# Kernel tuning notes

Hardware: AMD Instinct MI355X
Metric: run time of the kernel (lower is better)

Reference implementation:

```python
import jax, jax.numpy as jnp
import numpy as np

B, T, F, H = 64, 2048, 64, 160


def setup_inputs() -> dict:
    key = jax.random.key(0)
    ks = jax.random.split(key, 20)
    s = lambda *shape: 0.05
    inp = {
        "x": jax.random.normal(ks[0], (B, T, F), jnp.float32),
        # dilated conv weight [out=F, in=F, k=3]
        "mix_w": jax.random.normal(ks[1], (F, F, 3), jnp.float32) * 0.1,
        # batchnorm (inference) params
        "bn_g": jnp.ones((F,), jnp.float32),
        "bn_b": jnp.zeros((F,), jnp.float32),
        "bn_m": jax.random.normal(ks[2], (F,), jnp.float32) * 0.1,
        "bn_v": jax.random.uniform(ks[3], (F,), jnp.float32, 0.5, 1.5),
        # GRU1: input F -> hidden H (pytorch gate order r, z, n)
        "w_ih1": jax.random.normal(ks[4], (3 * H, F), jnp.float32) * 0.05,
        "w_hh1": jax.random.normal(ks[5], (3 * H, H), jnp.float32) * 0.05,
        "b_ih1": jax.random.normal(ks[6], (3 * H,), jnp.float32) * 0.05,
        "b_hh1": jax.random.normal(ks[7], (3 * H,), jnp.float32) * 0.05,
        # GRU2: hidden H -> hidden H
        "w_ih2": jax.random.normal(ks[8], (3 * H, H), jnp.float32) * 0.05,
        "w_hh2": jax.random.normal(ks[9], (3 * H, H), jnp.float32) * 0.05,
        "b_ih2": jax.random.normal(ks[10], (3 * H,), jnp.float32) * 0.05,
        "b_hh2": jax.random.normal(ks[11], (3 * H,), jnp.float32) * 0.05,
        # head: Linear(H, H//2) -> GELU -> (dropout=identity in eval) -> Linear(H//2, 2)
        "hw1": jax.random.normal(ks[12], (H // 2, H), jnp.float32) * 0.05,
        "hb1": jnp.zeros((H // 2,), jnp.float32),
        "hw2": jax.random.normal(ks[13], (2, H // 2), jnp.float32) * 0.05,
        "hb2": jnp.zeros((2,), jnp.float32),
    }
    return inp


def _gru(z, w_ih, w_hh, b_ih, b_hh):
    # z: [B, T, in]; returns (all hidden states [B, T, H], final hidden [B, H])
    xg = jnp.einsum('bti,gi->btg', z, w_ih) + b_ih  # [B, T, 3H]
    xg = xg.transpose(1, 0, 2)                       # [T, B, 3H]
    h0 = jnp.zeros((z.shape[0], w_hh.shape[1]), z.dtype)

    def step(h, g):
        hg = h @ w_hh.T + b_hh
        xr, xz, xn = jnp.split(g, 3, axis=-1)
        hr, hz, hn = jnp.split(hg, 3, axis=-1)
        r = jax.nn.sigmoid(xr + hr)
        u = jax.nn.sigmoid(xz + hz)
        n = jnp.tanh(xn + r * hn)
        h_new = (1.0 - u) * n + u * h
        return h_new, h_new

    hT, hs = jax.lax.scan(step, h0, xg)
    return hs.transpose(1, 0, 2), hT


def reference(x, mix_w, bn_g, bn_b, bn_m, bn_v,
              w_ih1, w_hh1, b_ih1, b_hh1,
              w_ih2, w_hh2, b_ih2, b_hh2,
              hw1, hb1, hw2, hb2):
    # dilated conv over time: x [B,T,F] -> [B,F,T]
    xc = x.transpose(0, 2, 1)
    y = jax.lax.conv_general_dilated(
        xc, mix_w, window_strides=(1,), padding=[(2, 2)],
        rhs_dilation=(2,), dimension_numbers=('NCH', 'OIH', 'NCH'))
    # batchnorm (inference) + exact GELU
    scale = bn_g / jnp.sqrt(bn_v + 1e-5)
    y = (y - bn_m[:, None]) * scale[:, None] + bn_b[:, None]
    z = jax.nn.gelu(y, approximate=False).transpose(0, 2, 1)  # [B,T,F]

    h1, _ = _gru(z, w_ih1, w_hh1, b_ih1, b_hh1)    # [B,T,H]
    _, h2T = _gru(h1, w_ih2, w_hh2, b_ih2, b_hh2)  # [B,H] (last timestep)

    q = jax.nn.gelu(h2T @ hw1.T + hb1, approximate=False)
    return q @ hw2.T + hb2  # [B, 2]
```

## Files before the change

### kernel.cpp

```cpp
#include <hip/hip_runtime.h>
#include <cmath>

#define BB 64
#define TT 2048
#define FF 64
#define HH 160
#define G3 480
#define TC 128
#define NC (TT / TC)

#define L2E  1.44269504088896340736f
#define TL2E 2.88539008177792681472f

typedef unsigned int u32;
typedef _Float16 half8 __attribute__((ext_vector_type(8)));
typedef _Float16 half2v __attribute__((ext_vector_type(2)));
typedef float f32x4 __attribute__((ext_vector_type(4)));

__device__ __forceinline__ unsigned short f2h(float v) {
    _Float16 h = (_Float16)v;
    return __builtin_bit_cast(unsigned short, h);
}
__device__ __forceinline__ u32 packh2(float a, float b) {
    return (u32)f2h(a) | ((u32)f2h(b) << 16);
}
__device__ __forceinline__ u32 packhh(_Float16 a, _Float16 b) {
    return (u32)__builtin_bit_cast(unsigned short, a)
         | ((u32)__builtin_bit_cast(unsigned short, b) << 16);
}
__device__ __forceinline__ float h2sel(u32 p, u32 sh) {
    return (float)__builtin_bit_cast(half2v, p >> sh)[0];
}
__device__ __forceinline__ float frcp(float v) { return __builtin_amdgcn_rcpf(v); }
#if __has_builtin(__builtin_amdgcn_exp2f)
__device__ __forceinline__ float fexp2(float v) { return __builtin_amdgcn_exp2f(v); }
#else
__device__ __forceinline__ float fexp2(float v) { return __expf(v * 0.69314718055994530942f); }
#endif
__device__ __forceinline__ float gelu_exact(float v) {
    return 0.5f * v * (1.f + erff(v * 0.70710678118654752f));
}
__device__ __forceinline__ void barrier_lgkm() {
    asm volatile("s_waitcnt lgkmcnt(0)\ns_barrier" ::: "memory");
}
__device__ __forceinline__ half8 load_wrow8s(const float* p, float s) {
    const float4* q = (const float4*)p;
    float4 a = q[0], b = q[1];
    half8 r;
    r[0] = (_Float16)(a.x * s); r[1] = (_Float16)(a.y * s);
    r[2] = (_Float16)(a.z * s); r[3] = (_Float16)(a.w * s);
    r[4] = (_Float16)(b.x * s); r[5] = (_Float16)(b.y * s);
    r[6] = (_Float16)(b.z * s); r[7] = (_Float16)(b.w * s);
    return r;
}
__device__ __forceinline__ void split8(const float* v, half8& hi, half8& lo) {
    #pragma unroll
    for (int j = 0; j < 8; ++j) {
        _Float16 h = (_Float16)v[j];
        hi[j] = h;
        lo[j] = (_Float16)(v[j] - (float)h);
    }
}
#define MM16(A_, B_, C_) __builtin_amdgcn_mfma_f32_16x16x32_f16(A_, B_, C_, 0, 0, 0)

__global__ __launch_bounds__(256) void conv_mfma_kernel(
    const float* __restrict__ x, const float* __restrict__ mix_w,
    const float* __restrict__ bn_g, const float* __restrict__ bn_b,
    const float* __restrict__ bn_m, const float* __restrict__ bn_v,
    u32* __restrict__ z_out)
{
    __shared__ __align__(16) u32 xs[68 * 68];
    __shared__ __align__(8)  u32 zt[16 * 34];

    const int b   = blockIdx.y;
    const int t0  = blockIdx.x * 64;
    const int tid = threadIdx.x;
    const int wv = tid >> 6;
    const int lane = tid & 63;
    const int lane15 = lane & 15;
    const int quad = lane >> 4;

    {
        const float* xb = x + (size_t)b * TT * FF;
        for (int idx = tid; idx < 68 * 32; idx += 256) {
            const int row = idx >> 5;
            const int fp  = (idx & 31) * 2;
            const int t = t0 - 2 + row;
            float v0 = 0.f, v1 = 0.f;
            if (t >= 0 && t < TT) {
                float2 v = *(const float2*)(xb + (size_t)t * FF + fp);
                v0 = v.x; v1 = v.y;
            }
            _Float16 h0 = (_Float16)v0, h1 = (_Float16)v1;
            _Float16 l0 = (_Float16)(v0 - (float)h0);
            _Float16 l1 = (_Float16)(v1 - (float)h1);
            u32* rw = xs + row * 68;
            rw[(fp >> 1)]      = packhh(h0, h1);
            rw[32 + (fp >> 1)] = packhh(l0, l1);
        }
    }

    half8 Ahi[6], Alo[6];
    {
        const int fo = wv * 16 + lane15;
        const float* wrow = mix_w + fo * 192;
        #pragma unroll
        for (int s = 0; s < 6; ++s) {
            float wf[8];
            #pragma unroll
            for (int j = 0; j < 8; ++j) {
                int kap = s * 32 + quad * 8 + j;
                wf[j] = wrow[(kap & 63) * 3 + (kap >> 6)];
            }
            split8(wf, Ahi[s], Alo[s]);
        }
    }
    float sc[4], sh[4];
    #pragma unroll
    for (int r = 0; r < 4; ++r) {
        int f = wv * 16 + quad * 4 + r;
        float scl = bn_g[f] * rsqrtf(bn_v[f] + 1e-5f);
        sc[r] = scl; sh[r] = bn_b[f] - bn_m[f] * scl;
    }

    __syncthreads();

    u32* zrow = z_out + (size_t)(b >> 4) * TT * 512 + (b & 15) * 32;
    const int srow = tid >> 4;
    const int sc2  = tid & 15;

    for (int tt = 0; tt < 4; ++tt) {
        f32x4 C = {0.f, 0.f, 0.f, 0.f};
        #pragma unroll
        for (int s = 0; s < 6; ++s) {
            const int row = tt * 16 + lane15 + 2 * (s >> 1);
            const u32* rp = xs + row * 68 + (s & 1) * 16 + quad * 4;
            half8 Bhi = __builtin_bit_cast(half8, *(const uint4*)(rp));
            half8 Blo = __builtin_bit_cast(half8, *(const uint4*)(rp + 32));
            C = MM16(Ahi[s], Bhi, C);
            C = MM16(Ahi[s], Blo, C);
            C = MM16(Alo[s], Bhi, C);
        }
        float z0 = gelu_exact(fmaf(C[0], sc[0], sh[0]));
        float z1 = gelu_exact(fmaf(C[1], sc[1], sh[1]));
        float z2 = gelu_exact(fmaf(C[2], sc[2], sh[2]));
        float z3 = gelu_exact(fmaf(C[3], sc[3], sh[3]));
        const u32 q0 = packh2(z0, z1);
        const u32 q1 = packh2(z2, z3);
        __syncthreads();
        *(uint2*)(zt + lane15 * 34 + wv * 8 + quad * 2) = (uint2){q0, q1};
        __syncthreads();
        uint2 v = *(const uint2*)(zt + srow * 34 + sc2 * 2);
        *(uint2*)(zrow + (size_t)(t0 + tt * 16 + srow) * 512 + sc2 * 2) = v;
    }
}

#define DECLAI(i) half8 A##i##_0, A##i##_1, A##i##_2, A##i##_3, A##i##_4;
#define GLOADA(i) { int tl = wv4 + (i); int rowc = tl < 30 ? tl * 16 + lane15 : 479; \
    float sA = tl < 20 ? L2E : TL2E;                                                 \
    const float* wp = W + (size_t)rowc * K + quad * 8;                               \
    A##i##_0 = load_wrow8s(wp, sA); A##i##_1 = load_wrow8s(wp + 32, sA);             \
    if (KT > 2) { A##i##_2 = load_wrow8s(wp + 64, sA);                               \
                  A##i##_3 = load_wrow8s(wp + 96, sA);                               \
                  A##i##_4 = load_wrow8s(wp + 128, sA); }                            \
    else { A##i##_2 = A##i##_0; A##i##_3 = A##i##_0; A##i##_4 = A##i##_0; } }
#define GMM(i, kt) C##i = MM16(A##i##_##kt, Bk##kt, C##i);

template<int K, int KT, int TG>
__device__ __forceinline__ void gemm_body(
    const unsigned short* __restrict__ in,
    size_t in_blk_stride, int t_off,
    const float* __restrict__ W, const float* __restrict__ b_ih,
    const float* __restrict__ b_hh, u32* __restrict__ xg,
    int gidx, int tid)
{
    if (tid >= 512) return;
    const int wv4 = (tid >> 6) * 4;
    const int lane = tid & 63;
    const int lane15 = lane & 15;
    const int quad = lane >> 4;
    const int blk = gidx >> 4;
    const int tbase = (gidx & 15) * TG;

    DECLAI(0) DECLAI(1) DECLAI(2) DECLAI(3)
    GLOADA(0) GLOADA(1) GLOADA(2) GLOADA(3)

    f32x4 BIAS0, BIAS1, BIAS2, BIAS3;
    #define GBIAS(i) { int tl = wv4 + (i); int rowb = tl < 30 ? tl * 16 + quad * 4 : 476; \
        float sB = tl < 20 ? L2E : TL2E;                                                  \
        float4 bi = *(const float4*)(b_ih + rowb);                                        \
        if (tl < 20) { float4 bh = *(const float4*)(b_hh + rowb);                         \
            bi.x += bh.x; bi.y += bh.y; bi.z += bh.z; bi.w += bh.w; }                     \
        BIAS##i[0] = bi.x * sB; BIAS##i[1] = bi.y * sB;                                   \
        BIAS##i[2] = bi.z * sB; BIAS##i[3] = bi.w * sB; }
    GBIAS(0) GBIAS(1) GBIAS(2) GBIAS(3)
    #undef GBIAS

    const unsigned short* inb = in + (size_t)blk * in_blk_stride;
    u32* xgb = xg + (size_t)blk * TC * 3840;

    for (int t = 0; t < TG; ++t) {
        const int tt = tbase + t;
        const unsigned short* ip =
            inb + ((size_t)(t_off + tt) * 16 + lane15) * K + quad * 8;
        half8 Bk0 = __builtin_bit_cast(half8, *(const uint4*)(ip));
        half8 Bk1 = __builtin_bit_cast(half8, *(const uint4*)(ip + 32));
        half8 Bk2 = Bk0, Bk3 = Bk0, Bk4 = Bk0;
        if (KT > 2) {
            Bk2 = __builtin_bit_cast(half8, *(const uint4*)(ip + 64));
            Bk3 = __builtin_bit_cast(half8, *(const uint4*)(ip + 96));
            Bk4 = __builtin_bit_cast(half8, *(const uint4*)(ip + 128));
        }
        f32x4 C0 = BIAS0, C1 = BIAS1, C2 = BIAS2, C3 = BIAS3;
        GMM(0, 0) GMM(1, 0) GMM(2, 0) GMM(3, 0)
        GMM(0, 1) GMM(1, 1) GMM(2, 1) GMM(3, 1)
        if (KT > 2) {
            GMM(0, 2) GMM(1, 2) GMM(2, 2) GMM(3, 2)
            GMM(0, 3) GMM(1, 3) GMM(2, 3) GMM(3, 3)
            GMM(0, 4) GMM(1, 4) GMM(2, 4) GMM(3, 4)
        }
        #define GSTORE(i) { int tl = wv4 + (i); if (tl < 30) {                      \
            u32 q0 = packh2(C##i[0], C##i[1]);                                      \
            u32 q1 = packh2(C##i[2], C##i[3]);                                      \
            *(uint2*)(xgb + (((size_t)tt * 30 + tl) * 16 + lane15) * 8 + quad * 2)  \
                = (uint2){q0, q1}; } }
        GSTORE(0) GSTORE(1) GSTORE(2) GSTORE(3)
        #undef GSTORE
    }
}

#define DECLW(nm) half8 nm##0, nm##1, nm##2, nm##3, nm##4;
#define LOADWHS(nm, tb, S) { const float* wp = w_hh + (size_t)((tb) * 16 + lane15) * HH + quad * 8; \
    nm##0 = load_wrow8s(wp, S);       nm##1 = load_wrow8s(wp + 32, S);                              \
    nm##2 = load_wrow8s(wp + 64, S);  nm##3 = load_wrow8s(wp + 96, S);                              \
    nm##4 = load_wrow8s(wp + 128, S); }

template<bool WRITE_H>
__device__ __forceinline__ void scan_body(
    const u32* __restrict__ xg,
    const float* __restrict__ w_hh, const float* __restrict__ b_hh,
    float* __restrict__ h_state,
    u32* __restrict__ h_out32,
    int first, int blk, int sub, int tid, u32* h_lds32)
{
    const int wv = tid >> 6;
    const int lane = tid & 63;
    const int lane15 = lane & 15;
    const int quad = lane >> 4;
    const int ch   = lane15 & 3;
    const int dup  = lane15 >> 2;
    const int ch0  = sub * 4;
    const int row_g = wv * 16 + quad * 4 + dup;
    const u32 shamt = (u32)(16 * (dup & 1));
    const bool d1 = (dup & 1) != 0;
    const bool d2 = (dup & 2) != 0;

    DECLW(Ar) DECLW(Az) DECLW(An)
    LOADWHS(Ar, wv, L2E) LOADWHS(Az, 10 + wv, L2E) LOADWHS(An, 20 + wv, TL2E)

    const float bh = b_hh[320 + row_g] * TL2E;

    float* hsp = h_state + (size_t)(blk * 16 + ch0 + ch) * HH + row_g;
    float ho = first ? 0.f : *hsp;

    const int widx = ch * 208 + row_g;
    unsigned short* hw16 = (unsigned short*)h_lds32;
    unsigned short* HW0 = hw16 + widx;
    unsigned short* HW1 = hw16 + 832 + widx;
    *HW0 = f2h(ho);

    const int vb = ch * 26 + quad;

    const u32* xgb = xg + (size_t)blk * TC * 3840;
    const int pr = quad * 2 + (dup >> 1);
    const int xo_r = ((wv)      * 16 + ch0 + ch) * 8 + pr;
    const int xo_z = ((10 + wv) * 16 + ch0 + ch) * 8 + pr;
    const int xo_n = ((20 + wv) * 16 + ch0 + ch) * 8 + pr;

    u32 xrP0 = xgb[0 * 3840 + xo_r], xzP0 = xgb[0 * 3840 + xo_z], xnP0 = xgb[0 * 3840 + xo_n];
    u32 xrP1 = xgb[1 * 3840 + xo_r], xzP1 = xgb[1 * 3840 + xo_z], xnP1 = xgb[1 * 3840 + xo_n];
    u32 xrP2 = xgb[2 * 3840 + xo_r], xzP2 = xgb[2 * 3840 + xo_z], xnP2 = xgb[2 * 3840 + xo_n];
    u32 xrP3 = xgb[3 * 3840 + xo_r], xzP3 = xgb[3 * 3840 + xo_z], xnP3 = xgb[3 * 3840 + xo_n];
    const u32* pf_r = xgb + 4 * 3840 + xo_r;
    const u32* pf_z = xgb + 4 * 3840 + xo_z;
    const u32* pf_n = xgb + 4 * 3840 + xo_n;

    unsigned short* hp = WRITE_H
            ? (unsigned short*)h_out32 + (size_t)blk * TC * 2560
              + (size_t)(ch0 + ch) * 160 + row_g
            : nullptr;
    __syncthreads();

    #define SCAN_STEP(RBOFF, HWP, XR, XZ, XN, PFO, HPO)                              \
    {                                                                                \
        const uint4* hb = (const uint4*)(h_lds32 + (RBOFF));                         \
        uint4 b0 = hb[vb];      uint4 b1 = hb[vb + 4];                               \
        uint4 b2 = hb[vb + 8];  uint4 b3 = hb[vb + 12];                              \
        uint4 b4 = hb[vb + 16];                                                      \
        float xrv = h2sel(XR, shamt);                                                \
        float xzv = h2sel(XZ, shamt);                                                \
        float xnv = h2sel(XN, shamt);                                                \
        f32x4 Cr = {xrv, xrv, xrv, xrv};                                             \
        f32x4 Cz = {xzv, xzv, xzv, xzv};                                             \
        f32x4 Cn = {bh, bh, bh, bh};                                                 \
        XR = pf_r[PFO]; XZ = pf_z[PFO]; XN = pf_n[PFO];                              \
        half8 B0 = __builtin_bit_cast(half8, b0);                                    \
        Cr = MM16(Ar0, B0, Cr); Cz = MM16(Az0, B0, Cz); Cn = MM16(An0, B0, Cn);      \
        half8 B1 = __builtin_bit_cast(half8, b1);                                    \
        Cr = MM16(Ar1, B1, Cr); Cz = MM16(Az1, B1, Cz); Cn = MM16(An1, B1, Cn);      \
        half8 B2 = __builtin_bit_cast(half8, b2);                                    \
        Cr = MM16(Ar2, B2, Cr); Cz = MM16(Az2, B2, Cz); Cn = MM16(An2, B2, Cn);      \
        half8 B3 = __builtin_bit_cast(half8, b3);                                    \
        Cr = MM16(Ar3, B3, Cr); Cz = MM16(Az3, B3, Cz); Cn = MM16(An3, B3, Cn);      \
        half8 B4 = __builtin_bit_cast(half8, b4);                                    \
        Cr = MM16(Ar4, B4, Cr); Cz = MM16(Az4, B4, Cz); Cn = MM16(An4, B4, Cn);      \
        {                                                                            \
            float ca = d1 ? Cr[1] : Cr[0];                                           \
            float cb = d1 ? Cr[3] : Cr[2];                                           \
            float crv = d2 ? cb : ca;                                                \
            ca = d1 ? Cz[1] : Cz[0];                                                 \
            cb = d1 ? Cz[3] : Cz[2];                                                 \
            float czv = d2 ? cb : ca;                                                \
            ca = d1 ? Cn[1] : Cn[0];                                                 \
            cb = d1 ? Cn[3] : Cn[2];                                                 \
            float cnv = d2 ? cb : ca;                                                \
            float r = frcp(1.f + fexp2(-crv));                                       \
            float u = frcp(1.f + fexp2(-czv));                                       \
            float e = fexp2(fmaf(r, cnv, xnv));                                      \
            float n = fmaf(-2.f, frcp(e + 1.f), 1.f);                                \
            ho = fmaf(u, ho - n, n);                                                 \
        }                                                                            \
        const unsigned short hv = f2h(ho);                                           \
        *(HWP) = hv;                                                                 \
        if (WRITE_H) { hp[HPO] = hv; }                                               \
        barrier_lgkm();                                                              \
    }

    for (int t4 = 0; t4 < TC; t4 += 4) {
        SCAN_STEP(0,   HW1, xrP0, xzP0, xnP0, 0 * 3840, 0 * 2560)
        SCAN_STEP(416, HW0, xrP1, xzP1, xnP1, 1 * 3840, 1 * 2560)
        SCAN_STEP(0,   HW1, xrP2, xzP2, xnP2, 2 * 3840, 2 * 2560)
        SCAN_STEP(416, HW0, xrP3, xzP3, xnP3, 3 * 3840, 3 * 2560)
        pf_r += 4 * 3840; pf_z += 4 * 3840; pf_n += 4 * 3840;
        if (WRITE_H) hp += 4 * 2560;
    }
    #undef SCAN_STEP

    *hsp = ho;
}

__global__ __launch_bounds__(640, 1) void pipe_stage(
    const u32* __restrict__ z,
    u32* __restrict__ xg1,
    u32* __restrict__ xg2,
    u32* __restrict__ h1c,
    float* __restrict__ h1s, float* __restrict__ h2s,
    const float* __restrict__ w_ih1, const float* __restrict__ b_ih1,
    const float* __restrict__ w_hh1, const float* __restrict__ b_hh1,
    const float* __restrict__ w_ih2, const float* __restrict__ b_ih2,
    const float* __restrict__ w_hh2, const float* __restrict__ b_hh2,
    int k)
{
    __shared__ __align__(16) u32 h_lds32[2 * 416];
    const int bx = blockIdx.x;
    const int tid = threadIdx.x;
    const size_t XGCH = (size_t)4 * TC * 3840;
    const size_t H1CH = (size_t)4 * TC * 1280;

    if (bx < 16) {
        const int c = k - 1;
        if (c < 0 || c >= NC) return;
        scan_body<true>(xg1 + (c & 1) * XGCH, w_hh1, b_hh1, h1s,
                        h1c + (c & 1) * H1CH, c == 0, bx >> 2, bx & 3, tid, h_lds32);
    } else if (bx < 32) {
        const int c = k - 3;
        if (c < 0 || c >= NC) return;
        scan_body<false>(xg2 + (c & 1) * XGCH, w_hh2, b_hh2, h2s,
                         nullptr, c == 0, (bx - 16) >> 2, (bx - 16) & 3, tid, h_lds32);
    } else if (bx < 96) {
        const int c = k;
        if (c >= NC) return;
        gemm_body<64, 2, 8>((const unsigned short*)z, (size_t)TT * 1024, c * TC,
                            w_ih1, b_ih1, b_hh1, xg1 + (c & 1) * XGCH, bx - 32, tid);
    } else {
        const int c = k - 2;
        if (c < 0 || c >= NC) return;
        gemm_body<160, 5, 8>((const unsigned short*)(h1c + (c & 1) * H1CH),
                             (size_t)TC * 2560, 0,
                             w_ih2, b_ih2, b_hh2, xg2 + (c & 1) * XGCH, bx - 96, tid);
    }
}

__global__ __launch_bounds__(256) void head_kernel(
    const float* __restrict__ h_state,
    const float* __restrict__ hw1, const float* __restrict__ hb1,
    const float* __restrict__ hw2, const float* __restrict__ hb2,
    float* __restrict__ out)
{
    const int b = blockIdx.x;
    const int tid = threadIdx.x;
    __shared__ float hf[HH];
    __shared__ float q[80];
    if (tid < HH) hf[tid] = h_state[b * HH + tid];
    __syncthreads();
    if (tid < 80) {
        float a = hb1[tid];
        const float* wr = hw1 + (size_t)tid * HH;
        #pragma unroll 8
        for (int i = 0; i < HH; ++i) a = fmaf(wr[i], hf[i], a);
        q[tid] = gelu_exact(a);
    }
    __syncthreads();
    if (tid < 2) {
        float o = hb2[tid];
        const float* wr = hw2 + tid * 80;
        #pragma unroll 8
        for (int j = 0; j < 80; ++j) o = fmaf(wr[j], q[j], o);
        out[b * 2 + tid] = o;
    }
}

extern "C" void kernel_launch(void* const* d_in, const int* in_sizes, int n_in,
                              void* d_out, int out_size, void* d_ws, size_t ws_size,
                              hipStream_t stream)
{
    const float* x     = (const float*)d_in[0];
    const float* mix_w = (const float*)d_in[1];
    const float* bn_g  = (const float*)d_in[2];
    const float* bn_b  = (const float*)d_in[3];
    const float* bn_m  = (const float*)d_in[4];
    const float* bn_v  = (const float*)d_in[5];
    const float* w_ih1 = (const float*)d_in[6];
    const float* w_hh1 = (const float*)d_in[7];
    const float* b_ih1 = (const float*)d_in[8];
    const float* b_hh1 = (const float*)d_in[9];
    const float* w_ih2 = (const float*)d_in[10];
    const float* w_hh2 = (const float*)d_in[11];
    const float* b_ih2 = (const float*)d_in[12];
    const float* b_hh2 = (const float*)d_in[13];
    const float* hw1   = (const float*)d_in[14];
    const float* hb1   = (const float*)d_in[15];
    const float* hw2   = (const float*)d_in[16];
    const float* hb2   = (const float*)d_in[17];
    float* out = (float*)d_out;

    char* p = (char*)d_ws;
    u32* z_ws  = (u32*)p;  p += (size_t)BB * TT * 32 * 4;
    u32* xg1_ws = (u32*)p; p += (size_t)2 * 4 * TC * 3840 * 4;
    u32* xg2_ws = (u32*)p; p += (size_t)2 * 4 * TC * 3840 * 4;
    u32* h1c_ws = (u32*)p; p += (size_t)2 * 4 * TC * 1280 * 4;
    float* h1s = (float*)p; p += (size_t)BB * HH * 4;
    float* h2s = (float*)p;

    conv_mfma_kernel<<<dim3(32, BB), 256, 0, stream>>>(
        x, mix_w, bn_g, bn_b, bn_m, bn_v, z_ws);

    for (int k = 0; k <= NC + 2; ++k) {
        pipe_stage<<<160, 640, 0, stream>>>(
            z_ws, xg1_ws, xg2_ws, h1c_ws, h1s, h2s,
            w_ih1, b_ih1, w_hh1, b_hh1,
            w_ih2, b_ih2, w_hh2, b_hh2, k);
    }

    head_kernel<<<BB, 256, 0, stream>>>(h2s, hw1, hb1, hw2, hb2, out);
}
```

Baseline: 1.621 ms.

## Halve pipeline stage granularity and reorder GRU step MFMAs for overlap

The staged GEMM/scan pipeline now advances in 64-timestep half-chunks over 35 launches instead of 128-timestep chunks over 19. This shrinks the fill and drain bubbles on the serial scan critical path, in exchange for more kernel launches and barriers. Inside each recurrent step, the MFMAs are grouped per gate (r, then n, then z) and the activation math is interleaved. The r and n nonlinearities can then start while the z-gate MFMAs are still running, which shortens per-step latency.

```diff
diff --git a/kernel.cpp b/kernel.cpp
--- a/kernel.cpp
+++ b/kernel.cpp
@@ -8,6 +8,7 @@
 #define G3 480
 #define TC 128
 #define NC (TT / TC)
+#define NHS 35
 
 #define L2E  1.44269504088896340736f
 #define TL2E 2.88539008177792681472f
@@ -42,6 +43,11 @@
 }
 __device__ __forceinline__ void barrier_lgkm() {
     asm volatile("s_waitcnt lgkmcnt(0)\ns_barrier" ::: "memory");
+}
+__device__ __forceinline__ float csel(f32x4 C, bool d1, bool d2) {
+    float ca = d1 ? C[1] : C[0];
+    float cb = d1 ? C[3] : C[2];
+    return d2 ? cb : ca;
 }
 __device__ __forceinline__ half8 load_wrow8s(const float* p, float s) {
     const float4* q = (const float4*)p;
@@ -172,7 +178,7 @@
     size_t in_blk_stride, int t_off,
     const float* __restrict__ W, const float* __restrict__ b_ih,
     const float* __restrict__ b_hh, u32* __restrict__ xg,
-    int gidx, int tid)
+    int gidx, int h, int tid)
 {
     if (tid >= 512) return;
     const int wv4 = (tid >> 6) * 4;
@@ -180,7 +186,7 @@
     const int lane15 = lane & 15;
     const int quad = lane >> 4;
     const int blk = gidx >> 4;
-    const int tbase = (gidx & 15) * TG;
+    const int tbase = (gidx & 15) * TG + h * 64;
 
     DECLAI(0) DECLAI(1) DECLAI(2) DECLAI(3)
     GLOADA(0) GLOADA(1) GLOADA(2) GLOADA(3)
@@ -241,7 +247,7 @@
     const float* __restrict__ w_hh, const float* __restrict__ b_hh,
     float* __restrict__ h_state,
     u32* __restrict__ h_out32,
-    int first, int blk, int sub, int tid, u32* h_lds32)
+    int first, int blk, int sub, int h, int tid, u32* h_lds32)
 {
     const int wv = tid >> 6;
     const int lane = tid & 63;
@@ -271,7 +277,7 @@
 
     const int vb = ch * 26 + quad;
 
-    const u32* xgb = xg + (size_t)blk * TC * 3840;
+    const u32* xgb = xg + (size_t)blk * TC * 3840 + (size_t)h * 64 * 3840;
     const int pr = quad * 2 + (dup >> 1);
     const int xo_r = ((wv)      * 16 + ch0 + ch) * 8 + pr;
     const int xo_z = ((10 + wv) * 16 + ch0 + ch) * 8 + pr;
@@ -287,7 +293,7 @@
 
     unsigned short* hp = WRITE_H
             ? (unsigned short*)h_out32 + (size_t)blk * TC * 2560
-              + (size_t)(ch0 + ch) * 160 + row_g
+              + (size_t)h * 64 * 2560 + (size_t)(ch0 + ch) * 160 + row_g
             : nullptr;
     __syncthreads();
 
@@ -305,38 +311,31 @@
         f32x4 Cn = {bh, bh, bh, bh};                                                 \
         XR = pf_r[PFO]; XZ = pf_z[PFO]; XN = pf_n[PFO];                              \
         half8 B0 = __builtin_bit_cast(half8, b0);                                    \
-        Cr = MM16(Ar0, B0, Cr); Cz = MM16(Az0, B0, Cz); Cn = MM16(An0, B0, Cn);      \
         half8 B1 = __builtin_bit_cast(half8, b1);                                    \
-        Cr = MM16(Ar1, B1, Cr); Cz = MM16(Az1, B1, Cz); Cn = MM16(An1, B1, Cn);      \
         half8 B2 = __builtin_bit_cast(half8, b2);                                    \
-        Cr = MM16(Ar2, B2, Cr); Cz = MM16(Az2, B2, Cz); Cn = MM16(An2, B2, Cn);      \
         half8 B3 = __builtin_bit_cast(half8, b3);                                    \
-        Cr = MM16(Ar3, B3, Cr); Cz = MM16(Az3, B3, Cz); Cn = MM16(An3, B3, Cn);      \
         half8 B4 = __builtin_bit_cast(half8, b4);                                    \
-        Cr = MM16(Ar4, B4, Cr); Cz = MM16(Az4, B4, Cz); Cn = MM16(An4, B4, Cn);      \
-        {                                                                            \
-            float ca = d1 ? Cr[1] : Cr[0];                                           \
-            float cb = d1 ? Cr[3] : Cr[2];                                           \
-            float crv = d2 ? cb : ca;                                                \
-            ca = d1 ? Cz[1] : Cz[0];                                                 \
-            cb = d1 ? Cz[3] : Cz[2];                                                 \
-            float czv = d2 ? cb : ca;                                                \
-            ca = d1 ? Cn[1] : Cn[0];                                                 \
-            cb = d1 ? Cn[3] : Cn[2];                                                 \
-            float cnv = d2 ? cb : ca;                                                \
-            float r = frcp(1.f + fexp2(-crv));                                       \
-            float u = frcp(1.f + fexp2(-czv));                                       \
-            float e = fexp2(fmaf(r, cnv, xnv));                                      \
-            float n = fmaf(-2.f, frcp(e + 1.f), 1.f);                                \
-            ho = fmaf(u, ho - n, n);                                                 \
-        }                                                                            \
+        Cr = MM16(Ar0, B0, Cr); Cr = MM16(Ar1, B1, Cr); Cr = MM16(Ar2, B2, Cr);      \
+        Cr = MM16(Ar3, B3, Cr); Cr = MM16(Ar4, B4, Cr);                              \
+        Cn = MM16(An0, B0, Cn); Cn = MM16(An1, B1, Cn); Cn = MM16(An2, B2, Cn);      \
+        Cn = MM16(An3, B3, Cn); Cn = MM16(An4, B4, Cn);                              \
+        Cz = MM16(Az0, B0, Cz); Cz = MM16(Az1, B1, Cz); Cz = MM16(Az2, B2, Cz);      \
+        Cz = MM16(Az3, B3, Cz); Cz = MM16(Az4, B4, Cz);                              \
+        float crv = csel(Cr, d1, d2);                                                \
+        float r = frcp(1.f + fexp2(-crv));                                           \
+        float cnv = csel(Cn, d1, d2);                                                \
+        float e = fexp2(fmaf(r, cnv, xnv));                                          \
+        float n = fmaf(-2.f, frcp(e + 1.f), 1.f);                                    \
+        float czv = csel(Cz, d1, d2);                                                \
+        float u = frcp(1.f + fexp2(-czv));                                           \
+        ho = fmaf(u, ho - n, n);                                                     \
         const unsigned short hv = f2h(ho);                                           \
         *(HWP) = hv;                                                                 \
         if (WRITE_H) { hp[HPO] = hv; }                                               \
         barrier_lgkm();                                                              \
     }
 
-    for (int t4 = 0; t4 < TC; t4 += 4) {
+    for (int t4 = 0; t4 < 64; t4 += 4) {
         SCAN_STEP(0,   HW1, xrP0, xzP0, xnP0, 0 * 3840, 0 * 2560)
         SCAN_STEP(416, HW0, xrP1, xzP1, xnP1, 1 * 3840, 1 * 2560)
         SCAN_STEP(0,   HW1, xrP2, xzP2, xnP2, 2 * 3840, 2 * 2560)
@@ -359,7 +358,7 @@
     const float* __restrict__ w_hh1, const float* __restrict__ b_hh1,
     const float* __restrict__ w_ih2, const float* __restrict__ b_ih2,
     const float* __restrict__ w_hh2, const float* __restrict__ b_hh2,
-    int k)
+    int hs)
 {
     __shared__ __align__(16) u32 h_lds32[2 * 416];
     const int bx = blockIdx.x;
@@ -368,26 +367,30 @@
     const size_t H1CH = (size_t)4 * TC * 1280;
 
     if (bx < 16) {
-        const int c = k - 1;
-        if (c < 0 || c >= NC) return;
+        const int u = hs - 1;
+        if (u < 0 || u >= 32) return;
+        const int c = u >> 1, h = u & 1;
         scan_body<true>(xg1 + (c & 1) * XGCH, w_hh1, b_hh1, h1s,
-                        h1c + (c & 1) * H1CH, c == 0, bx >> 2, bx & 3, tid, h_lds32);
+                        h1c + (c & 1) * H1CH, u == 0, bx >> 2, bx & 3, h, tid, h_lds32);
     } else if (bx < 32) {
-        const int c = k - 3;
-        if (c < 0 || c >= NC) return;
+        const int u = hs - 3;
+        if (u < 0 || u >= 32) return;
+        const int c = u >> 1, h = u & 1;
         scan_body<false>(xg2 + (c & 1) * XGCH, w_hh2, b_hh2, h2s,
-                         nullptr, c == 0, (bx - 16) >> 2, (bx - 16) & 3, tid, h_lds32);
+                         nullptr, u == 0, (bx - 16) >> 2, (bx - 16) & 3, h, tid, h_lds32);
     } else if (bx < 96) {
-        const int c = k;
-        if (c >= NC) return;
-        gemm_body<64, 2, 8>((const unsigned short*)z, (size_t)TT * 1024, c * TC,
-                            w_ih1, b_ih1, b_hh1, xg1 + (c & 1) * XGCH, bx - 32, tid);
+        const int u = hs;
+        if (u >= 32) return;
+        const int c = u >> 1, h = u & 1;
+        gemm_body<64, 2, 4>((const unsigned short*)z, (size_t)TT * 1024, c * TC,
+                            w_ih1, b_ih1, b_hh1, xg1 + (c & 1) * XGCH, bx - 32, h, tid);
     } else {
-        const int c = k - 2;
-        if (c < 0 || c >= NC) return;
-        gemm_body<160, 5, 8>((const unsigned short*)(h1c + (c & 1) * H1CH),
+        const int u = hs - 2;
+        if (u < 0 || u >= 32) return;
+        const int c = u >> 1, h = u & 1;
+        gemm_body<160, 5, 4>((const unsigned short*)(h1c + (c & 1) * H1CH),
                              (size_t)TC * 2560, 0,
-                             w_ih2, b_ih2, b_hh2, xg2 + (c & 1) * XGCH, bx - 96, tid);
+                             w_ih2, b_ih2, b_hh2, xg2 + (c & 1) * XGCH, bx - 96, h, tid);
     }
 }
 
@@ -455,11 +458,11 @@
     conv_mfma_kernel<<<dim3(32, BB), 256, 0, stream>>>(
         x, mix_w, bn_g, bn_b, bn_m, bn_v, z_ws);
 
-    for (int k = 0; k <= NC + 2; ++k) {
+    for (int hs = 0; hs < NHS; ++hs) {
         pipe_stage<<<160, 640, 0, stream>>>(
             z_ws, xg1_ws, xg2_ws, h1c_ws, h1s, h2s,
             w_ih1, b_ih1, w_hh1, b_hh1,
-            w_ih2, b_ih2, w_hh2, b_hh2, k);
+            w_ih2, b_ih2, w_hh2, b_hh2, hs);
     }
 
     head_kernel<<<BB, 256, 0, stream>>>(h2s, hw1, hb1, hw2, hb2, out);
```

Result: slower. 1.722 ms (+6.2%).
